# Performance work log

Measured on AMD Instinct MI355X. Metric: run time of the kernel, lower is better.

The kernel has to match this reference:

```python
import jax, jax.numpy as jnp
import numpy as np
from jax import lax

B, N, C = 16, 2000, 81
MAX_INST = 100
MIN_CONF = 0.7
NMS_THR = 0.3
BBOX_STD = jnp.array([0.1, 0.1, 0.2, 0.2], jnp.float32)
IMG_H = IMG_W = 1024
NEG = -1e9


def setup_inputs() -> dict:
    key = jax.random.key(0)
    k1, k2, k3 = jax.random.split(key, 3)
    # rois: normalized boxes with y1<y2, x1<x2
    yx = jax.random.uniform(k1, (B, N, 2, 2), dtype=jnp.float32)
    y = jnp.sort(yx[..., 0], axis=-1)
    x = jnp.sort(yx[..., 1], axis=-1)
    rois = jnp.stack([y[..., 0], x[..., 0], y[..., 1], x[..., 1]], axis=-1)
    # class probabilities (softmax over classes); temperature makes some scores pass 0.7
    mrcnn_class = jax.nn.softmax(3.0 * jax.random.normal(k2, (B, N, C), dtype=jnp.float32), axis=-1)
    mrcnn_bbox = 0.1 * jax.random.normal(k3, (B, N, C, 4), dtype=jnp.float32)
    # image_meta: [image_id(1), original_shape(3), image_shape(3), window(4), scale(1), active_class_ids(C)]
    meta = np.zeros((B, 12 + C), np.float32)
    meta[:, 1:4] = [IMG_H, IMG_W, 3]
    meta[:, 4:7] = [IMG_H, IMG_W, 3]
    meta[:, 7:11] = [0, 0, IMG_H, IMG_W]
    meta[:, 11] = 1.0
    return {"rois": rois, "mrcnn_class": mrcnn_class, "mrcnn_bbox": mrcnn_bbox,
            "image_meta": jnp.asarray(meta)}


def _apply_deltas(boxes, deltas):
    h = boxes[:, 2] - boxes[:, 0]
    w = boxes[:, 3] - boxes[:, 1]
    cy = boxes[:, 0] + 0.5 * h
    cx = boxes[:, 1] + 0.5 * w
    cy = cy + deltas[:, 0] * h
    cx = cx + deltas[:, 1] * w
    h = h * jnp.exp(deltas[:, 2])
    w = w * jnp.exp(deltas[:, 3])
    return jnp.stack([cy - 0.5 * h, cx - 0.5 * w, cy + 0.5 * h, cx + 0.5 * w], axis=-1)


def _iou_row(box, boxes):
    y1 = jnp.maximum(box[0], boxes[:, 0])
    x1 = jnp.maximum(box[1], boxes[:, 1])
    y2 = jnp.minimum(box[2], boxes[:, 2])
    x2 = jnp.minimum(box[3], boxes[:, 3])
    inter = jnp.maximum(y2 - y1, 0.0) * jnp.maximum(x2 - x1, 0.0)
    a1 = (box[2] - box[0]) * (box[3] - box[1])
    a2 = (boxes[:, 2] - boxes[:, 0]) * (boxes[:, 3] - boxes[:, 1])
    return inter / (a1 + a2 - inter + 1e-12)


def _refine_one(rois, probs, deltas, window):
    # rois [N,4], probs [N,C], deltas [N,C,4], window [4]
    idx = jnp.arange(N)
    class_ids = jnp.argmax(probs, axis=1)                 # [N]
    scores = probs[idx, class_ids]                        # [N]
    d = deltas[idx, class_ids] * BBOX_STD                 # [N,4]
    boxes = _apply_deltas(rois, d)
    wy1, wx1, wy2, wx2 = window[0], window[1], window[2], window[3]
    boxes = jnp.stack([jnp.clip(boxes[:, 0], wy1, wy2),
                       jnp.clip(boxes[:, 1], wx1, wx2),
                       jnp.clip(boxes[:, 2], wy1, wy2),
                       jnp.clip(boxes[:, 3], wx1, wx2)], axis=-1)
    # filter background and low confidence
    kept = (class_ids > 0) & (scores >= MIN_CONF)
    masked_scores = jnp.where(kept, scores, NEG)
    order = jnp.argsort(-masked_scores)                   # descending by score
    b = boxes[order]
    c = class_ids[order]
    s = masked_scores[order]
    suppressed0 = ~kept[order]

    def body(i, sup):
        iou = _iou_row(b[i], b)                           # [N]
        kill = (iou > NMS_THR) & (c == c[i]) & (idx > i) & (~sup[i])
        return sup | kill

    sup = lax.fori_loop(0, N, body, suppressed0)          # class-wise greedy NMS
    final = jnp.where(sup, NEG, s)
    top_s, top_i = lax.top_k(final, MAX_INST)             # global top detections
    det = jnp.concatenate([b[top_i],
                           c[top_i, None].astype(jnp.float32),
                           top_s[:, None]], axis=-1)      # [MAX_INST, 6]
    valid = top_s >= MIN_CONF
    return jnp.where(valid[:, None], det, 0.0)            # zero-pad invalid rows


def reference(rois, mrcnn_class, mrcnn_bbox, image_meta):
    image_shape = image_meta[0, 4:7]
    window = image_meta[:, 7:11]                          # [B,4] in pixels
    h, w = image_shape[0], image_shape[1]
    scale = jnp.stack([h - 1.0, w - 1.0, h - 1.0, w - 1.0])
    shift = jnp.array([0.0, 0.0, 1.0, 1.0], jnp.float32)
    norm_window = (window - shift) / scale                # norm_boxes_graph
    dets = jax.vmap(_refine_one)(rois, mrcnn_class, mrcnn_bbox, norm_window)
    return dets.reshape(B, MAX_INST, 6)
```

## Files before the change

### kernel.cpp

```cpp
#include <hip/hip_runtime.h>

#define NB    16
#define NN    2000
#define NC    81
#define NPAD  2048
#define MAXI  100
#define MINC  0.7f
#define NMST  0.3f
#define NEGV  -1000000000.0f
#define BTP   256
#define BT    512
#define NWAVE (BT/64)

#define WS_BOX_OFF  0
#define WS_KEY_OFF  (NB * NN * 16)
#define WS_NEEDED   (WS_KEY_OFF + NB * NN * 8)

__device__ __forceinline__ unsigned ordf(float f) {
    unsigned u = __float_as_uint(f);
    return (u & 0x80000000u) ? ~u : (u | 0x80000000u);
}
__device__ __forceinline__ float unordf(unsigned u) {
    unsigned b = (u & 0x80000000u) ? (u ^ 0x80000000u) : ~u;
    return __uint_as_float(b);
}

__device__ __forceinline__ unsigned long long cx64(unsigned long long k, int j,
                                                   bool desc, int lane) {
    unsigned lo = __shfl_xor((unsigned)k, j, 64);
    unsigned hi = __shfl_xor((unsigned)(k >> 32), j, 64);
    unsigned long long p = ((unsigned long long)hi << 32) | lo;
    bool lower    = ((lane & j) == 0);
    bool take_max = (lower == desc);
    return ((p > k) == take_max) ? p : k;
}


__global__ __launch_bounds__(BTP)
void prep_kernel(const float* __restrict__ rois,
                 const float* __restrict__ probs,
                 const float* __restrict__ deltas,
                 const float* __restrict__ meta,
                 float4* __restrict__ wbox,
                 unsigned long long* __restrict__ wkey) {
    const int g = threadIdx.x >> 4;
    const int l = threadIdx.x & 15;
    const int r = blockIdx.x * 16 + g;
    const int b = r / NN;
    const int i = r - b * NN;

    const float* prow = probs + (size_t)r * NC;
    float best = -1.0f; int cb = 0;
    for (int c = l; c < NC; c += 16) {
        float p = prow[c];
        if (p > best) { best = p; cb = c; }
    }
    #pragma unroll
    for (int off = 8; off; off >>= 1) {
        float pb = __shfl_xor(best, off, 16);
        int   co = __shfl_xor(cb,   off, 16);
        if (pb > best || (pb == best && co < cb)) { best = pb; cb = co; }
    }

    if (l == 0) {
        const int MS = 12 + NC;
        const float ih = meta[4], iw = meta[5];
        const float sy = ih - 1.0f, sx = iw - 1.0f;
        const float wy1 = (meta[(size_t)b * MS + 7]        ) / sy;
        const float wx1 = (meta[(size_t)b * MS + 8]        ) / sx;
        const float wy2 = (meta[(size_t)b * MS + 9]  - 1.0f) / sy;
        const float wx2 = (meta[(size_t)b * MS + 10] - 1.0f) / sx;

        const float* drow = deltas + ((size_t)r * NC + cb) * 4;
        float dy = drow[0] * 0.1f, dx = drow[1] * 0.1f;
        float dh = drow[2] * 0.2f, dw = drow[3] * 0.2f;

        const float4 r4 = *(const float4*)(rois + (size_t)r * 4);
        float h  = r4.z - r4.x;
        float w  = r4.w - r4.y;
        float cy = r4.x + 0.5f * h;
        float cx = r4.y + 0.5f * w;
        cy = cy + dy * h;
        cx = cx + dx * w;
        h  = h * expf(dh);
        w  = w * expf(dw);
        float y1 = fminf(fmaxf(cy - 0.5f * h, wy1), wy2);
        float x1 = fminf(fmaxf(cx - 0.5f * w, wx1), wx2);
        float y2 = fminf(fmaxf(cy + 0.5f * h, wy1), wy2);
        float x2 = fminf(fmaxf(cx + 0.5f * w, wx1), wx2);

        wbox[r] = make_float4(y1, x1, y2, x2);
        bool kept = (cb > 0) && (best >= MINC);
        float msc = kept ? best : NEGV;
        wkey[r] = ((unsigned long long)ordf(msc) << 32)
                | (unsigned long long)(((unsigned)(2047 - i) << 8) | (unsigned)cb);
    }
}

__global__ __launch_bounds__(BT)
void det2_kernel(const float4* __restrict__ wbox,
                 const unsigned long long* __restrict__ wkey,
                 float* __restrict__ out) {
    __shared__ unsigned long long skey[NPAD];
    __shared__ float4 sboxR[NPAD];
    __shared__ unsigned char sup[NPAD];
    __shared__ unsigned short pool[NPAD];
    __shared__ int hist[82], cstart[82], cnt[82];
    __shared__ int out_rank[MAXI];
    __shared__ int sK, nsurv;

    const int b    = blockIdx.x;
    const int tid  = threadIdx.x;
    const int lane = tid & 63;
    const int wv   = tid >> 6;

    for (int c = tid; c < 82; c += BT) { hist[c] = 0; cnt[c] = 0; }
    if (tid == 0) { sK = 0; nsurv = 0; }
    __syncthreads();

    const unsigned minc_ord = ordf(MINC);
    for (int base = 0; base < NN; base += BT) {
        int i = base + tid;
        unsigned long long k = 0ull; bool kept = false;
        if (i < NN) {
            k = wkey[(size_t)b * NN + i];
            kept = ((unsigned)(k >> 32) >= minc_ord);
        }
        unsigned long long m = __ballot(kept);
        int c64 = __popcll(m);
        int basep = 0;
        if (lane == 0 && c64) basep = atomicAdd(&sK, c64);
        basep = __shfl(basep, 0, 64);
        if (kept) skey[basep + __popcll(m & ((1ull << lane) - 1))] = k;
    }
    __syncthreads();
    const int K = sK;
    int P = 0;
    if (K > 0) { P = 64; while (P < K) P <<= 1; }
    for (int t = K + tid; t < P; t += BT) skey[t] = 0ull;
    __syncthreads();

    if (P > 0 && P <= 64 * NWAVE) {
        const int nch = P >> 6;
        const int e   = (wv << 6) + lane;
        unsigned long long k = 0ull;
        if (wv < nch) {
            k = skey[e];
            #pragma unroll
            for (int kk2 = 2; kk2 <= 64; kk2 <<= 1) {
                #pragma unroll
                for (int j = 32; j; j >>= 1) {
                    if (j < kk2) k = cx64(k, j, ((e & kk2) == 0), lane);
                }
            }
            skey[e] = k;
        }
        __syncthreads();
        for (int kk = 128; kk <= P; kk <<= 1) {
            for (int j = kk >> 1; j >= 64; j >>= 1) {
                int jm = j - 1;
                for (int p = tid; p < (P >> 1); p += BT) {
                    int t  = ((p & ~jm) << 1) | (p & jm);
                    int ix = t + j;
                    unsigned long long a = skey[t], c2 = skey[ix];
                    bool desc = ((t & kk) == 0);
                    if ((a < c2) == desc) { skey[t] = c2; skey[ix] = a; }
                }
                __syncthreads();
            }
            if (wv < nch) {
                k = skey[e];
                const bool desc = ((e & kk) == 0);
                #pragma unroll
                for (int j = 32; j; j >>= 1) k = cx64(k, j, desc, lane);
                skey[e] = k;
            }
            __syncthreads();
        }
    } else if (P > 0) {
        for (int kk = 2; kk <= P; kk <<= 1) {
            for (int j = kk >> 1; j > 0; j >>= 1) {
                int jm = j - 1;
                for (int p = tid; p < (P >> 1); p += BT) {
                    int t  = ((p & ~jm) << 1) | (p & jm);
                    int ix = t + j;
                    unsigned long long a = skey[t], c2 = skey[ix];
                    bool desc = ((t & kk) == 0);
                    if ((a < c2) == desc) { skey[t] = c2; skey[ix] = a; }
                }
                __syncthreads();
            }
        }
    }

    for (int r2 = tid; r2 < K; r2 += BT) {
        unsigned low = (unsigned)(skey[r2] & 0xFFFFFFFFull);
        int oi = 2047 - (int)((low >> 8) & 0x7FF);
        sboxR[r2] = wbox[(size_t)b * NN + oi];
        sup[r2] = 0;
        atomicAdd(&hist[low & 0xFF], 1);
    }
    __syncthreads();

    if (wv == 0) {
        int c0 = 2 * lane, c1 = c0 + 1;
        int h0 = (c0 < 82) ? hist[c0] : 0;
        int h1 = (c1 < 82) ? hist[c1] : 0;
        int s = h0 + h1, sc = s;
        #pragma unroll
        for (int off = 1; off < 64; off <<= 1) {
            int v = __shfl_up(sc, off, 64);
            if (lane >= off) sc += v;
        }
        int excl = sc - s;
        if (c0 < 82) cstart[c0] = excl;
        if (c1 < 82) cstart[c1] = excl + h0;
    }
    __syncthreads();

    if (wv == 0) {
        for (int chunk = 0; chunk < K; chunk += 64) {
            int r2 = chunk + lane;
            bool v = r2 < K;
            int c = v ? (int)(skey[r2] & 0xFF) : 127;
            unsigned long long m = ~0ull;
            #pragma unroll
            for (int kb = 0; kb < 7; ++kb) {
                unsigned long long bk = __ballot((c >> kb) & 1);
                m &= ((c >> kb) & 1) ? bk : ~bk;
            }
            int leader = __ffsll(m) - 1;
            int before = __popcll(m & ((1ull << lane) - 1));
            int basec = 0;
            if (v && lane == leader) basec = atomicAdd(&cnt[c], __popcll(m));
            basec = __shfl(basec, leader, 64);
            if (v) pool[cstart[c] + basec + before] = (unsigned short)r2;
        }
    }
    __syncthreads();

    for (int c = 1 + wv; c < 82; c += NWAVE) {
        int s0 = cstart[c], n = hist[c];
        if (n <= 1) continue;
        if (n <= 64) {
            int ri = 0; float4 bi = make_float4(0.f,0.f,0.f,0.f);
            float ai = 0.f; bool alive = false;
            if (lane < n) {
                ri = pool[s0 + lane];
                bi = sboxR[ri];
                ai = (bi.z - bi.x) * (bi.w - bi.y);
                alive = true;
            }
            unsigned long long cand = __ballot(alive);
            while (cand) {
                int curl = __ffsll(cand) - 1;
                float cy1 = __shfl(bi.x, curl, 64);
                float cx1 = __shfl(bi.y, curl, 64);
                float cy2 = __shfl(bi.z, curl, 64);
                float cx2 = __shfl(bi.w, curl, 64);
                float ca  = __shfl(ai,  curl, 64);
                float yy1 = fmaxf(cy1, bi.x);
                float xx1 = fmaxf(cx1, bi.y);
                float yy2 = fminf(cy2, bi.z);
                float xx2 = fminf(cx2, bi.w);
                float inter = fmaxf(yy2 - yy1, 0.0f) * fmaxf(xx2 - xx1, 0.0f);
                float iou = inter / (ca + ai - inter + 1e-12f);
                bool kill = alive && (lane > curl) && (iou > NMST);
                unsigned long long km = __ballot(kill);
                if (kill) alive = false;
                cand &= ~km;
                cand &= ~(1ull << curl);
            }
            if (lane < n && !alive) sup[ri] = 1;
        } else {
            volatile unsigned char* vsup = sup;
            for (int ii = 0; ii < n; ++ii) {
                int ri = pool[s0 + ii];
                if (vsup[ri]) continue;
                float4 bi = sboxR[ri];
                float ai = (bi.z - bi.x) * (bi.w - bi.y);
                for (int jj = ii + 1 + lane; jj < n; jj += 64) {
                    int rj = pool[s0 + jj];
                    float4 bj = sboxR[rj];
                    float yy1 = fmaxf(bi.x, bj.x);
                    float xx1 = fmaxf(bi.y, bj.y);
                    float yy2 = fminf(bi.z, bj.z);
                    float xx2 = fminf(bi.w, bj.w);
                    float inter = fmaxf(yy2 - yy1, 0.0f) * fmaxf(xx2 - xx1, 0.0f);
                    float aj = (bj.z - bj.x) * (bj.w - bj.y);
                    float iou = inter / (ai + aj - inter + 1e-12f);
                    if (iou > NMST) vsup[rj] = 1;
                }
            }
        }
    }
    __syncthreads();

    if (wv == 0) {
        int total = 0;
        for (int chunk = 0; chunk < K && total < MAXI; chunk += 64) {
            int r2 = chunk + lane;
            bool alivex = (r2 < K) && !sup[r2];
            unsigned long long m = __ballot(alivex);
            int pos = total + __popcll(m & ((1ull << lane) - 1));
            if (alivex && pos < MAXI) out_rank[pos] = r2;
            total += __popcll(m);
        }
        if (lane == 0) nsurv = total < MAXI ? total : MAXI;
    }
    __syncthreads();

    const int ns = nsurv;
    for (int o = tid; o < MAXI; o += BT) {
        float v0=0.f,v1=0.f,v2=0.f,v3=0.f,v4=0.f,v5=0.f;
        if (o < ns) {
            int r2 = out_rank[o];
            float4 bo = sboxR[r2];
            unsigned long long kr = skey[r2];
            v0 = bo.x; v1 = bo.y; v2 = bo.z; v3 = bo.w;
            v4 = (float)(int)(kr & 0xFF);
            v5 = unordf((unsigned)(kr >> 32));
        }
        float* op = out + ((size_t)b * MAXI + o) * 6;
        op[0]=v0; op[1]=v1; op[2]=v2; op[3]=v3; op[4]=v4; op[5]=v5;
    }
}

__global__ __launch_bounds__(256)
void det_mono_kernel(const float* __restrict__ rois,
                     const float* __restrict__ probs,
                     const float* __restrict__ deltas,
                     const float* __restrict__ meta,
                     float* __restrict__ out) {
    __shared__ unsigned long long key[NPAD];
    __shared__ float4 sbox[NN];
    __shared__ unsigned char scls[NN];
    __shared__ unsigned char sup[NPAD];
    __shared__ int out_rank[MAXI];
    __shared__ int sK;
    __shared__ int nsurv;

    const int b   = blockIdx.x;
    const int tid = threadIdx.x;
    const int MSTRIDE = 12 + NC;

    if (tid == 0) { sK = 0; nsurv = 0; }

    const float ih = meta[4], iw = meta[5];
    const float sy = ih - 1.0f, sx = iw - 1.0f;
    const float wy1 = (meta[(size_t)b * MSTRIDE + 7]) / sy;
    const float wx1 = (meta[(size_t)b * MSTRIDE + 8]) / sx;
    const float wy2 = (meta[(size_t)b * MSTRIDE + 9] - 1.0f) / sy;
    const float wx2 = (meta[(size_t)b * MSTRIDE + 10] - 1.0f) / sx;

    for (int i = tid; i < NN; i += 256) {
        const float* prow = probs + ((size_t)b * NN + i) * NC;
        float best = prow[0];
        int cb = 0;
        #pragma unroll
        for (int c = 1; c < NC; ++c) {
            float p = prow[c];
            if (p > best) { best = p; cb = c; }
        }
        const float* drow = deltas + (((size_t)b * NN + i) * NC + cb) * 4;
        float dy = drow[0] * 0.1f, dx = drow[1] * 0.1f;
        float dh = drow[2] * 0.2f, dw = drow[3] * 0.2f;
        const float4 r4 = *(const float4*)(rois + ((size_t)b * NN + i) * 4);
        float h  = r4.z - r4.x;
        float w  = r4.w - r4.y;
        float cy = r4.x + 0.5f * h;
        float cx = r4.y + 0.5f * w;
        cy = cy + dy * h;
        cx = cx + dx * w;
        h  = h * expf(dh);
        w  = w * expf(dw);
        float y1 = fminf(fmaxf(cy - 0.5f * h, wy1), wy2);
        float x1 = fminf(fmaxf(cx - 0.5f * w, wx1), wx2);
        float y2 = fminf(fmaxf(cy + 0.5f * h, wy1), wy2);
        float x2 = fminf(fmaxf(cx + 0.5f * w, wx1), wx2);
        sbox[i] = make_float4(y1, x1, y2, x2);
        scls[i] = (unsigned char)cb;
        bool kept = (cb > 0) && (best >= MINC);
        float msc = kept ? best : NEGV;
        key[i] = ((unsigned long long)ordf(msc) << 32)
               | (unsigned long long)(0xFFFFFFFFu - (unsigned)i);
    }
    for (int i = NN + tid; i < NPAD; i += 256) key[i] = 0ull;
    __syncthreads();

    for (int k = 2; k <= NPAD; k <<= 1) {
        for (int j = k >> 1; j > 0; j >>= 1) {
            for (int t = tid; t < NPAD; t += 256) {
                int ix = t ^ j;
                if (ix > t) {
                    unsigned long long a = key[t], c = key[ix];
                    bool descend = ((t & k) == 0);
                    if ((a < c) == descend) { key[t] = c; key[ix] = a; }
                }
            }
            __syncthreads();
        }
    }

    const unsigned minc_ord = ordf(MINC);
    for (int r = tid; r < NPAD; r += 256) {
        unsigned su = (unsigned)(key[r] >> 32);
        bool kept = (su >= minc_ord);
        sup[r] = kept ? 0 : 1;
        if (kept) atomicAdd(&sK, 1);
    }
    __syncthreads();
    const int K = sK;

    for (int i = 0; i < K; ++i) {
        __syncthreads();
        if (nsurv >= MAXI) break;
        if (sup[i]) continue;
        unsigned long long ki = key[i];
        int oi = (int)(0xFFFFFFFFu - (unsigned)(ki & 0xFFFFFFFFull));
        float4 bi = sbox[oi];
        int ci = scls[oi];
        float ai = (bi.z - bi.x) * (bi.w - bi.y);
        for (int jr = i + 1 + tid; jr < K; jr += 256) {
            int oj = (int)(0xFFFFFFFFu - (unsigned)(key[jr] & 0xFFFFFFFFull));
            if ((int)scls[oj] != ci) continue;
            float4 bj = sbox[oj];
            float yy1 = fmaxf(bi.x, bj.x);
            float xx1 = fmaxf(bi.y, bj.y);
            float yy2 = fminf(bi.z, bj.z);
            float xx2 = fminf(bi.w, bj.w);
            float inter = fmaxf(yy2 - yy1, 0.0f) * fmaxf(xx2 - xx1, 0.0f);
            float aj = (bj.z - bj.x) * (bj.w - bj.y);
            float iou = inter / (ai + aj - inter + 1e-12f);
            if (iou > NMST) sup[jr] = 1;
        }
        if (tid == 0) { out_rank[nsurv] = i; nsurv += 1; }
    }
    __syncthreads();

    const int ns = nsurv;
    for (int o = tid; o < MAXI; o += 256) {
        float v0=0.f,v1=0.f,v2=0.f,v3=0.f,v4=0.f,v5=0.f;
        if (o < ns) {
            int r = out_rank[o];
            unsigned long long kr = key[r];
            int orr = (int)(0xFFFFFFFFu - (unsigned)(kr & 0xFFFFFFFFull));
            float4 bo = sbox[orr];
            v0 = bo.x; v1 = bo.y; v2 = bo.z; v3 = bo.w;
            v4 = (float)scls[orr];
            v5 = unordf((unsigned)(kr >> 32));
        }
        float* op = out + ((size_t)b * MAXI + o) * 6;
        op[0]=v0; op[1]=v1; op[2]=v2; op[3]=v3; op[4]=v4; op[5]=v5;
    }
}

extern "C" void kernel_launch(void* const* d_in, const int* in_sizes, int n_in,
                              void* d_out, int out_size, void* d_ws, size_t ws_size,
                              hipStream_t stream) {
    const float* rois   = (const float*)d_in[0];
    const float* probs  = (const float*)d_in[1];
    const float* deltas = (const float*)d_in[2];
    const float* meta   = (const float*)d_in[3];
    float* out = (float*)d_out;
    (void)in_sizes; (void)n_in; (void)out_size;

    if (ws_size >= (size_t)WS_NEEDED) {
        char* ws = (char*)d_ws;
        float4* wbox = (float4*)(ws + WS_BOX_OFF);
        unsigned long long* wkey = (unsigned long long*)(ws + WS_KEY_OFF);
        prep_kernel<<<(NB * NN) / 16, BTP, 0, stream>>>(rois, probs, deltas, meta,
                                                        wbox, wkey);
        det2_kernel<<<NB, BT, 0, stream>>>(wbox, wkey, out);
    } else {
        det_mono_kernel<<<NB, 256, 0, stream>>>(rois, probs, deltas, meta, out);
    }
}
```

Before: 29.48 us.

## Parallelize class bucketing and compaction across waves, load boxes during compaction

Boxes are now read together with keys in the initial compaction pass and stored in compacted order. The key embeds the compacted slot index so boxes are reached by indirection, which removes the post-sort gather from global memory. The serial single-wave class bucketing and survivor compaction are replaced by per-chunk histograms and prefix scans spread across all waves. The fallback for large candidate counts now uses a multi-chunk per-wave sort instead of the pure shared-memory bitonic sort. This adds more barriers and shared-memory scans, and the key packing changes, which needs the index bits not to collide.

Result: slower. 30.94 us (+5.0%).

```diff
diff --git a/kernel.cpp b/kernel.cpp
--- a/kernel.cpp
+++ b/kernel.cpp
@@ -4,6 +4,7 @@
 #define NN    2000
 #define NC    81
 #define NPAD  2048
+#define NCHMAX (NPAD/64)
 #define MAXI  100
 #define MINC  0.7f
 #define NMST  0.3f
@@ -93,7 +94,8 @@
         bool kept = (cb > 0) && (best >= MINC);
         float msc = kept ? best : NEGV;
         wkey[r] = ((unsigned long long)ordf(msc) << 32)
-                | (unsigned long long)(((unsigned)(2047 - i) << 8) | (unsigned)cb);
+                | ((unsigned long long)(unsigned)(2047 - i) << 21)
+                | (unsigned long long)(unsigned)cb;
     }
 }
 
@@ -102,10 +104,12 @@
                  const unsigned long long* __restrict__ wkey,
                  float* __restrict__ out) {
     __shared__ unsigned long long skey[NPAD];
-    __shared__ float4 sboxR[NPAD];
+    __shared__ float4 sboxC[NN];
     __shared__ unsigned char sup[NPAD];
     __shared__ unsigned short pool[NPAD];
-    __shared__ int hist[82], cstart[82], cnt[82];
+    __shared__ unsigned short chunkhist[NCHMAX][NC + 1];
+    __shared__ int hist[NC + 1], cstart[NC + 1];
+    __shared__ int chunkAlive[NCHMAX], chunkOff[NCHMAX];
     __shared__ int out_rank[MAXI];
     __shared__ int sK, nsurv;
 
@@ -114,38 +118,53 @@
     const int lane = tid & 63;
     const int wv   = tid >> 6;
 
-    for (int c = tid; c < 82; c += BT) { hist[c] = 0; cnt[c] = 0; }
+    for (int t = tid; t < (NCHMAX * (NC + 1)) / 2; t += BT)
+        ((unsigned*)&chunkhist[0][0])[t] = 0u;
+    for (int t = tid; t < NC + 1; t += BT) hist[t] = 0;
+    if (tid < NCHMAX) chunkAlive[tid] = 0;
     if (tid == 0) { sK = 0; nsurv = 0; }
     __syncthreads();
 
     const unsigned minc_ord = ordf(MINC);
-    for (int base = 0; base < NN; base += BT) {
-        int i = base + tid;
-        unsigned long long k = 0ull; bool kept = false;
+    unsigned long long kq[4]; float4 bq[4];
+    #pragma unroll
+    for (int q = 0; q < 4; ++q) {
+        int i = q * BT + tid;
         if (i < NN) {
-            k = wkey[(size_t)b * NN + i];
-            kept = ((unsigned)(k >> 32) >= minc_ord);
-        }
+            kq[q] = wkey[(size_t)b * NN + i];
+            bq[q] = wbox[(size_t)b * NN + i];
+        } else {
+            kq[q] = 0ull;
+            bq[q] = make_float4(0.f, 0.f, 0.f, 0.f);
+        }
+    }
+    #pragma unroll
+    for (int q = 0; q < 4; ++q) {
+        bool kept = ((unsigned)(kq[q] >> 32) >= minc_ord);
         unsigned long long m = __ballot(kept);
         int c64 = __popcll(m);
         int basep = 0;
         if (lane == 0 && c64) basep = atomicAdd(&sK, c64);
         basep = __shfl(basep, 0, 64);
-        if (kept) skey[basep + __popcll(m & ((1ull << lane) - 1))] = k;
-    }
-    __syncthreads();
+        if (kept) {
+            int pos = basep + __popcll(m & ((1ull << lane) - 1));
+            skey[pos]  = kq[q] | ((unsigned long long)((unsigned)pos << 10));
+            sboxC[pos] = bq[q];
+            atomicAdd(&hist[(int)(kq[q] & 0x7F)], 1);
+        }
+    }
+    __syncthreads();
+
     const int K = sK;
     int P = 0;
     if (K > 0) { P = 64; while (P < K) P <<= 1; }
     for (int t = K + tid; t < P; t += BT) skey[t] = 0ull;
     __syncthreads();
 
-    if (P > 0 && P <= 64 * NWAVE) {
-        const int nch = P >> 6;
-        const int e   = (wv << 6) + lane;
-        unsigned long long k = 0ull;
-        if (wv < nch) {
-            k = skey[e];
+    if (P > 0) {
+        for (int sb = wv << 6; sb < P; sb += (NWAVE << 6)) {
+            int e = sb + lane;
+            unsigned long long k = skey[e];
             #pragma unroll
             for (int kk2 = 2; kk2 <= 64; kk2 <<= 1) {
                 #pragma unroll
@@ -168,8 +187,9 @@
                 }
                 __syncthreads();
             }
-            if (wv < nch) {
-                k = skey[e];
+            for (int sb = wv << 6; sb < P; sb += (NWAVE << 6)) {
+                int e = sb + lane;
+                unsigned long long k = skey[e];
                 const bool desc = ((e & kk) == 0);
                 #pragma unroll
                 for (int j = 32; j; j >>= 1) k = cx64(k, j, desc, lane);
@@ -177,35 +197,30 @@
             }
             __syncthreads();
         }
-    } else if (P > 0) {
-        for (int kk = 2; kk <= P; kk <<= 1) {
-            for (int j = kk >> 1; j > 0; j >>= 1) {
-                int jm = j - 1;
-                for (int p = tid; p < (P >> 1); p += BT) {
-                    int t  = ((p & ~jm) << 1) | (p & jm);
-                    int ix = t + j;
-                    unsigned long long a = skey[t], c2 = skey[ix];
-                    bool desc = ((t & kk) == 0);
-                    if ((a < c2) == desc) { skey[t] = c2; skey[ix] = a; }
-                }
-                __syncthreads();
-            }
-        }
-    }
-
-    for (int r2 = tid; r2 < K; r2 += BT) {
-        unsigned low = (unsigned)(skey[r2] & 0xFFFFFFFFull);
-        int oi = 2047 - (int)((low >> 8) & 0x7FF);
-        sboxR[r2] = wbox[(size_t)b * NN + oi];
-        sup[r2] = 0;
-        atomicAdd(&hist[low & 0xFF], 1);
+    }
+
+    const int nch = (K + 63) >> 6;
+
+    for (int chunk = wv; chunk < nch; chunk += NWAVE) {
+        int r2 = (chunk << 6) + lane;
+        bool v = r2 < K;
+        int c = v ? (int)(skey[r2] & 0x7F) : 127;
+        if (v) sup[r2] = 0;
+        unsigned long long m = ~0ull;
+        #pragma unroll
+        for (int kb = 0; kb < 7; ++kb) {
+            unsigned long long bk = __ballot((c >> kb) & 1);
+            m &= ((c >> kb) & 1) ? bk : ~bk;
+        }
+        int leader = __ffsll(m) - 1;
+        if (v && lane == leader) chunkhist[chunk][c] = (unsigned short)__popcll(m);
     }
     __syncthreads();
 
     if (wv == 0) {
         int c0 = 2 * lane, c1 = c0 + 1;
-        int h0 = (c0 < 82) ? hist[c0] : 0;
-        int h1 = (c1 < 82) ? hist[c1] : 0;
+        int h0 = (c0 < NC + 1) ? hist[c0] : 0;
+        int h1 = (c1 < NC + 1) ? hist[c1] : 0;
         int s = h0 + h1, sc = s;
         #pragma unroll
         for (int off = 1; off < 64; off <<= 1) {
@@ -213,33 +228,39 @@
             if (lane >= off) sc += v;
         }
         int excl = sc - s;
-        if (c0 < 82) cstart[c0] = excl;
-        if (c1 < 82) cstart[c1] = excl + h0;
-    }
-    __syncthreads();
-
-    if (wv == 0) {
-        for (int chunk = 0; chunk < K; chunk += 64) {
-            int r2 = chunk + lane;
-            bool v = r2 < K;
-            int c = v ? (int)(skey[r2] & 0xFF) : 127;
-            unsigned long long m = ~0ull;
-            #pragma unroll
-            for (int kb = 0; kb < 7; ++kb) {
-                unsigned long long bk = __ballot((c >> kb) & 1);
-                m &= ((c >> kb) & 1) ? bk : ~bk;
-            }
-            int leader = __ffsll(m) - 1;
-            int before = __popcll(m & ((1ull << lane) - 1));
-            int basec = 0;
-            if (v && lane == leader) basec = atomicAdd(&cnt[c], __popcll(m));
-            basec = __shfl(basec, leader, 64);
-            if (v) pool[cstart[c] + basec + before] = (unsigned short)r2;
-        }
-    }
-    __syncthreads();
-
-    for (int c = 1 + wv; c < 82; c += NWAVE) {
+        if (c0 < NC + 1) cstart[c0] = excl;
+        if (c1 < NC + 1) cstart[c1] = excl + h0;
+    }
+    __syncthreads();
+
+    for (int c = wv; c < NC + 1; c += NWAVE) {
+        int v = (lane < NCHMAX) ? (int)chunkhist[lane][c] : 0;
+        int sc = v;
+        #pragma unroll
+        for (int off = 1; off < NCHMAX; off <<= 1) {
+            int u = __shfl_up(sc, off, 64);
+            if (lane >= off) sc += u;
+        }
+        if (lane < NCHMAX) chunkhist[lane][c] = (unsigned short)(sc - v);
+    }
+    __syncthreads();
+
+    for (int chunk = wv; chunk < nch; chunk += NWAVE) {
+        int r2 = (chunk << 6) + lane;
+        bool v = r2 < K;
+        int c = v ? (int)(skey[r2] & 0x7F) : 127;
+        unsigned long long m = ~0ull;
+        #pragma unroll
+        for (int kb = 0; kb < 7; ++kb) {
+            unsigned long long bk = __ballot((c >> kb) & 1);
+            m &= ((c >> kb) & 1) ? bk : ~bk;
+        }
+        int before = __popcll(m & ((1ull << lane) - 1));
+        if (v) pool[cstart[c] + (int)chunkhist[chunk][c] + before] = (unsigned short)r2;
+    }
+    __syncthreads();
+
+    for (int c = 1 + wv; c < NC + 1; c += NWAVE) {
         int s0 = cstart[c], n = hist[c];
         if (n <= 1) continue;
         if (n <= 64) {
@@ -247,7 +268,8 @@
             float ai = 0.f; bool alive = false;
             if (lane < n) {
                 ri = pool[s0 + lane];
-                bi = sboxR[ri];
+                unsigned long long kr = skey[ri];
+                bi = sboxC[(int)((kr >> 10) & 0x7FF)];
                 ai = (bi.z - bi.x) * (bi.w - bi.y);
                 alive = true;
             }
@@ -258,7 +280,7 @@
                 float cx1 = __shfl(bi.y, curl, 64);
                 float cy2 = __shfl(bi.z, curl, 64);
                 float cx2 = __shfl(bi.w, curl, 64);
-                float ca  = __shfl(ai,  curl, 64);
+                float ca  = (cy2 - cy1) * (cx2 - cx1);
                 float yy1 = fmaxf(cy1, bi.x);
                 float xx1 = fmaxf(cx1, bi.y);
                 float yy2 = fminf(cy2, bi.z);
@@ -277,11 +299,13 @@
             for (int ii = 0; ii < n; ++ii) {
                 int ri = pool[s0 + ii];
                 if (vsup[ri]) continue;
-                float4 bi = sboxR[ri];
+                unsigned long long kri = skey[ri];
+                float4 bi = sboxC[(int)((kri >> 10) & 0x7FF)];
                 float ai = (bi.z - bi.x) * (bi.w - bi.y);
                 for (int jj = ii + 1 + lane; jj < n; jj += 64) {
                     int rj = pool[s0 + jj];
-                    float4 bj = sboxR[rj];
+                    unsigned long long krj = skey[rj];
+                    float4 bj = sboxC[(int)((krj >> 10) & 0x7FF)];
                     float yy1 = fmaxf(bi.x, bj.x);
                     float xx1 = fmaxf(bi.y, bj.y);
                     float yy2 = fminf(bi.z, bj.z);
@@ -296,17 +320,31 @@
     }
     __syncthreads();
 
+    for (int chunk = wv; chunk < nch; chunk += NWAVE) {
+        int r2 = (chunk << 6) + lane;
+        bool alive = (r2 < K) && !sup[r2];
+        unsigned long long m = __ballot(alive);
+        if (lane == 0) chunkAlive[chunk] = __popcll(m);
+    }
+    __syncthreads();
     if (wv == 0) {
-        int total = 0;
-        for (int chunk = 0; chunk < K && total < MAXI; chunk += 64) {
-            int r2 = chunk + lane;
-            bool alivex = (r2 < K) && !sup[r2];
-            unsigned long long m = __ballot(alivex);
-            int pos = total + __popcll(m & ((1ull << lane) - 1));
-            if (alivex && pos < MAXI) out_rank[pos] = r2;
-            total += __popcll(m);
-        }
-        if (lane == 0) nsurv = total < MAXI ? total : MAXI;
+        int v = (lane < NCHMAX) ? chunkAlive[lane] : 0;
+        int sc = v;
+        #pragma unroll
+        for (int off = 1; off < NCHMAX; off <<= 1) {
+            int u = __shfl_up(sc, off, 64);
+            if (lane >= off) sc += u;
+        }
+        if (lane < NCHMAX) chunkOff[lane] = sc - v;
+        if (lane == NCHMAX - 1) nsurv = (sc < MAXI) ? sc : MAXI;
+    }
+    __syncthreads();
+    for (int chunk = wv; chunk < nch; chunk += NWAVE) {
+        int r2 = (chunk << 6) + lane;
+        bool alive = (r2 < K) && !sup[r2];
+        unsigned long long m = __ballot(alive);
+        int posn = chunkOff[chunk] + __popcll(m & ((1ull << lane) - 1));
+        if (alive && posn < MAXI) out_rank[posn] = r2;
     }
     __syncthreads();
 
@@ -315,10 +353,10 @@
         float v0=0.f,v1=0.f,v2=0.f,v3=0.f,v4=0.f,v5=0.f;
         if (o < ns) {
             int r2 = out_rank[o];
-            float4 bo = sboxR[r2];
             unsigned long long kr = skey[r2];
+            float4 bo = sboxC[(int)((kr >> 10) & 0x7FF)];
             v0 = bo.x; v1 = bo.y; v2 = bo.z; v3 = bo.w;
-            v4 = (float)(int)(kr & 0xFF);
+            v4 = (float)(int)(kr & 0x7F);
             v5 = unordf((unsigned)(kr >> 32));
         }
         float* op = out + ((size_t)b * MAXI + o) * 6;
```

## Fuse prep and detection kernels using last-block-done atomic counter per image

Applied to the files above, without the earlier changes.

Merges the per-ROI prep kernel into the detection kernel. Each image is split across 16 blocks that each compute argmax, decoded boxes and keys for 125 ROIs, then bump a per-image atomic counter. The last block to finish runs the sort/NMS/output stage. This removes one kernel launch and the gap between the kernels, but adds a hipMemsetAsync, threadfences, and a heavy 512-thread block with large shared memory for only the prep work, which reduces prep parallelism (4 lanes per row instead of 16).

Measured after the change: 73.13 us. +148.1%, slower.

```diff
diff --git a/kernel.cpp b/kernel.cpp
--- a/kernel.cpp
+++ b/kernel.cpp
@@ -8,13 +8,15 @@
 #define MINC  0.7f
 #define NMST  0.3f
 #define NEGV  -1000000000.0f
-#define BTP   256
 #define BT    512
 #define NWAVE (BT/64)
-
-#define WS_BOX_OFF  0
-#define WS_KEY_OFF  (NB * NN * 16)
-#define WS_NEEDED   (WS_KEY_OFF + NB * NN * 8)
+#define NBPI  16
+#define RPB   125
+
+#define WS_BOX_OFF   0
+#define WS_KEY_OFF   (NB * NN * 16)
+#define WS_DONE_OFF  (WS_KEY_OFF + NB * NN * 8)
+#define WS_NEEDED    (WS_DONE_OFF + 64)
 
 __device__ __forceinline__ unsigned ordf(float f) {
     unsigned u = __float_as_uint(f);
@@ -36,71 +38,15 @@
 }
 
 
-__global__ __launch_bounds__(BTP)
-void prep_kernel(const float* __restrict__ rois,
-                 const float* __restrict__ probs,
-                 const float* __restrict__ deltas,
-                 const float* __restrict__ meta,
-                 float4* __restrict__ wbox,
-                 unsigned long long* __restrict__ wkey) {
-    const int g = threadIdx.x >> 4;
-    const int l = threadIdx.x & 15;
-    const int r = blockIdx.x * 16 + g;
-    const int b = r / NN;
-    const int i = r - b * NN;
-
-    const float* prow = probs + (size_t)r * NC;
-    float best = -1.0f; int cb = 0;
-    for (int c = l; c < NC; c += 16) {
-        float p = prow[c];
-        if (p > best) { best = p; cb = c; }
-    }
-    #pragma unroll
-    for (int off = 8; off; off >>= 1) {
-        float pb = __shfl_xor(best, off, 16);
-        int   co = __shfl_xor(cb,   off, 16);
-        if (pb > best || (pb == best && co < cb)) { best = pb; cb = co; }
-    }
-
-    if (l == 0) {
-        const int MS = 12 + NC;
-        const float ih = meta[4], iw = meta[5];
-        const float sy = ih - 1.0f, sx = iw - 1.0f;
-        const float wy1 = (meta[(size_t)b * MS + 7]        ) / sy;
-        const float wx1 = (meta[(size_t)b * MS + 8]        ) / sx;
-        const float wy2 = (meta[(size_t)b * MS + 9]  - 1.0f) / sy;
-        const float wx2 = (meta[(size_t)b * MS + 10] - 1.0f) / sx;
-
-        const float* drow = deltas + ((size_t)r * NC + cb) * 4;
-        float dy = drow[0] * 0.1f, dx = drow[1] * 0.1f;
-        float dh = drow[2] * 0.2f, dw = drow[3] * 0.2f;
-
-        const float4 r4 = *(const float4*)(rois + (size_t)r * 4);
-        float h  = r4.z - r4.x;
-        float w  = r4.w - r4.y;
-        float cy = r4.x + 0.5f * h;
-        float cx = r4.y + 0.5f * w;
-        cy = cy + dy * h;
-        cx = cx + dx * w;
-        h  = h * expf(dh);
-        w  = w * expf(dw);
-        float y1 = fminf(fmaxf(cy - 0.5f * h, wy1), wy2);
-        float x1 = fminf(fmaxf(cx - 0.5f * w, wx1), wx2);
-        float y2 = fminf(fmaxf(cy + 0.5f * h, wy1), wy2);
-        float x2 = fminf(fmaxf(cx + 0.5f * w, wx1), wx2);
-
-        wbox[r] = make_float4(y1, x1, y2, x2);
-        bool kept = (cb > 0) && (best >= MINC);
-        float msc = kept ? best : NEGV;
-        wkey[r] = ((unsigned long long)ordf(msc) << 32)
-                | (unsigned long long)(((unsigned)(2047 - i) << 8) | (unsigned)cb);
-    }
-}
-
 __global__ __launch_bounds__(BT)
-void det2_kernel(const float4* __restrict__ wbox,
-                 const unsigned long long* __restrict__ wkey,
-                 float* __restrict__ out) {
+void fused_kernel(const float* __restrict__ rois,
+                  const float* __restrict__ probs,
+                  const float* __restrict__ deltas,
+                  const float* __restrict__ meta,
+                  float4* __restrict__ wbox,
+                  unsigned long long* __restrict__ wkey,
+                  unsigned int* __restrict__ done,
+                  float* __restrict__ out) {
     __shared__ unsigned long long skey[NPAD];
     __shared__ float4 sboxR[NPAD];
     __shared__ unsigned char sup[NPAD];
@@ -108,8 +54,78 @@
     __shared__ int hist[82], cstart[82], cnt[82];
     __shared__ int out_rank[MAXI];
     __shared__ int sK, nsurv;
-
-    const int b    = blockIdx.x;
+    __shared__ int amLast;
+
+    const int bi    = blockIdx.x;
+    const int b     = bi >> 4;
+    const int chunk = bi & (NBPI - 1);
+
+    {
+        const int t = threadIdx.x;
+        const int g = t >> 2;
+        const int l = t & 3;
+        if (g < RPB) {
+            const int i = chunk * RPB + g;
+            const size_t r = (size_t)b * NN + i;
+            const float* prow = probs + r * NC;
+            float best = -1.0f; int cb = 0;
+            for (int c = l; c < NC; c += 4) {
+                float p = prow[c];
+                if (p > best) { best = p; cb = c; }
+            }
+            #pragma unroll
+            for (int off = 1; off < 4; off <<= 1) {
+                float pb = __shfl_xor(best, off, 4);
+                int   co = __shfl_xor(cb,   off, 4);
+                if (pb > best || (pb == best && co < cb)) { best = pb; cb = co; }
+            }
+            if (l == 0) {
+                const int MS = 12 + NC;
+                const float ih = meta[4], iw = meta[5];
+                const float sy = ih - 1.0f, sx = iw - 1.0f;
+                const float wy1 = (meta[(size_t)b * MS + 7]        ) / sy;
+                const float wx1 = (meta[(size_t)b * MS + 8]        ) / sx;
+                const float wy2 = (meta[(size_t)b * MS + 9]  - 1.0f) / sy;
+                const float wx2 = (meta[(size_t)b * MS + 10] - 1.0f) / sx;
+
+                const float* drow = deltas + (r * NC + cb) * 4;
+                float dy = drow[0] * 0.1f, dx = drow[1] * 0.1f;
+                float dh = drow[2] * 0.2f, dw = drow[3] * 0.2f;
+
+                const float4 r4 = *(const float4*)(rois + r * 4);
+                float h  = r4.z - r4.x;
+                float w  = r4.w - r4.y;
+                float cy = r4.x + 0.5f * h;
+                float cx = r4.y + 0.5f * w;
+                cy = cy + dy * h;
+                cx = cx + dx * w;
+                h  = h * expf(dh);
+                w  = w * expf(dw);
+                float y1 = fminf(fmaxf(cy - 0.5f * h, wy1), wy2);
+                float x1 = fminf(fmaxf(cx - 0.5f * w, wx1), wx2);
+                float y2 = fminf(fmaxf(cy + 0.5f * h, wy1), wy2);
+                float x2 = fminf(fmaxf(cx + 0.5f * w, wx1), wx2);
+
+                wbox[r] = make_float4(y1, x1, y2, x2);
+                bool kept = (cb > 0) && (best >= MINC);
+                float msc = kept ? best : NEGV;
+                wkey[r] = ((unsigned long long)ordf(msc) << 32)
+                        | (unsigned long long)(((unsigned)(2047 - i) << 8)
+                                               | (unsigned)cb);
+            }
+        }
+    }
+
+    __threadfence();
+    __syncthreads();
+    if (threadIdx.x == 0) {
+        unsigned old = atomicAdd(&done[b], 1u);
+        amLast = (old == NBPI - 1) ? 1 : 0;
+        if (amLast) __threadfence();
+    }
+    __syncthreads();
+    if (!amLast) return;
+
     const int tid  = threadIdx.x;
     const int lane = tid & 63;
     const int wv   = tid >> 6;
@@ -219,8 +235,8 @@
     __syncthreads();
 
     if (wv == 0) {
-        for (int chunk = 0; chunk < K; chunk += 64) {
-            int r2 = chunk + lane;
+        for (int ch = 0; ch < K; ch += 64) {
+            int r2 = ch + lane;
             bool v = r2 < K;
             int c = v ? (int)(skey[r2] & 0xFF) : 127;
             unsigned long long m = ~0ull;
@@ -243,26 +259,26 @@
         int s0 = cstart[c], n = hist[c];
         if (n <= 1) continue;
         if (n <= 64) {
-            int ri = 0; float4 bi = make_float4(0.f,0.f,0.f,0.f);
+            int ri = 0; float4 bi2 = make_float4(0.f,0.f,0.f,0.f);
             float ai = 0.f; bool alive = false;
             if (lane < n) {
                 ri = pool[s0 + lane];
-                bi = sboxR[ri];
-                ai = (bi.z - bi.x) * (bi.w - bi.y);
+                bi2 = sboxR[ri];
+                ai = (bi2.z - bi2.x) * (bi2.w - bi2.y);
                 alive = true;
             }
             unsigned long long cand = __ballot(alive);
             while (cand) {
                 int curl = __ffsll(cand) - 1;
-                float cy1 = __shfl(bi.x, curl, 64);
-                float cx1 = __shfl(bi.y, curl, 64);
-                float cy2 = __shfl(bi.z, curl, 64);
-                float cx2 = __shfl(bi.w, curl, 64);
-                float ca  = __shfl(ai,  curl, 64);
-                float yy1 = fmaxf(cy1, bi.x);
-                float xx1 = fmaxf(cx1, bi.y);
-                float yy2 = fminf(cy2, bi.z);
-                float xx2 = fminf(cx2, bi.w);
+                float cy1 = __shfl(bi2.x, curl, 64);
+                float cx1 = __shfl(bi2.y, curl, 64);
+                float cy2 = __shfl(bi2.z, curl, 64);
+                float cx2 = __shfl(bi2.w, curl, 64);
+                float ca  = __shfl(ai,   curl, 64);
+                float yy1 = fmaxf(cy1, bi2.x);
+                float xx1 = fmaxf(cx1, bi2.y);
+                float yy2 = fminf(cy2, bi2.z);
+                float xx2 = fminf(cx2, bi2.w);
                 float inter = fmaxf(yy2 - yy1, 0.0f) * fmaxf(xx2 - xx1, 0.0f);
                 float iou = inter / (ca + ai - inter + 1e-12f);
                 bool kill = alive && (lane > curl) && (iou > NMST);
@@ -277,15 +293,15 @@
             for (int ii = 0; ii < n; ++ii) {
                 int ri = pool[s0 + ii];
                 if (vsup[ri]) continue;
-                float4 bi = sboxR[ri];
-                float ai = (bi.z - bi.x) * (bi.w - bi.y);
+                float4 bi2 = sboxR[ri];
+                float ai = (bi2.z - bi2.x) * (bi2.w - bi2.y);
                 for (int jj = ii + 1 + lane; jj < n; jj += 64) {
                     int rj = pool[s0 + jj];
                     float4 bj = sboxR[rj];
-                    float yy1 = fmaxf(bi.x, bj.x);
-                    float xx1 = fmaxf(bi.y, bj.y);
-                    float yy2 = fminf(bi.z, bj.z);
-                    float xx2 = fminf(bi.w, bj.w);
+                    float yy1 = fmaxf(bi2.x, bj.x);
+                    float xx1 = fmaxf(bi2.y, bj.y);
+                    float yy2 = fminf(bi2.z, bj.z);
+                    float xx2 = fminf(bi2.w, bj.w);
                     float inter = fmaxf(yy2 - yy1, 0.0f) * fmaxf(xx2 - xx1, 0.0f);
                     float aj = (bj.z - bj.x) * (bj.w - bj.y);
                     float iou = inter / (ai + aj - inter + 1e-12f);
@@ -298,8 +314,8 @@
 
     if (wv == 0) {
         int total = 0;
-        for (int chunk = 0; chunk < K && total < MAXI; chunk += 64) {
-            int r2 = chunk + lane;
+        for (int ch = 0; ch < K && total < MAXI; ch += 64) {
+            int r2 = ch + lane;
             bool alivex = (r2 < K) && !sup[r2];
             unsigned long long m = __ballot(alivex);
             int pos = total + __popcll(m & ((1ull << lane) - 1));
@@ -469,9 +485,10 @@
         char* ws = (char*)d_ws;
         float4* wbox = (float4*)(ws + WS_BOX_OFF);
         unsigned long long* wkey = (unsigned long long*)(ws + WS_KEY_OFF);
-        prep_kernel<<<(NB * NN) / 16, BTP, 0, stream>>>(rois, probs, deltas, meta,
-                                                        wbox, wkey);
-        det2_kernel<<<NB, BT, 0, stream>>>(wbox, wkey, out);
+        unsigned int* done = (unsigned int*)(ws + WS_DONE_OFF);
+        hipMemsetAsync(done, 0, 64, stream);
+        fused_kernel<<<NB * NBPI, BT, 0, stream>>>(rois, probs, deltas, meta,
+                                                   wbox, wkey, done, out);
     } else {
         det_mono_kernel<<<NB, 256, 0, stream>>>(rois, probs, deltas, meta, out);
     }
```
